# Optimization experiments

Measured on AMD Instinct MI355X. Metric: run time of the kernel, lower is better.

The kernel has to match this reference:

```python
import itertools
import jax, jax.numpy as jnp
import numpy as np

H, W = 512, 512
B, G, F, C = 2, 4, 9, 3
N = H * W


def _morton(pos):
    # pos: [N,3] int; interleave bits as in MortonFromPosition
    pos = np.asarray(pos, dtype=np.int32)
    code = np.zeros(len(pos), dtype=np.int64)
    coeff = np.asarray([4, 2, 1], dtype=np.int64)
    for b in range(21):
        code |= ((pos & (1 << b)) << (2 * b)) @ coeff
    return code


def _build_graph(h, w):
    xindex, yindex = np.meshgrid(np.arange(w), np.arange(h))
    xy = np.stack([yindex, xindex], axis=2).reshape(-1, 2)
    z = np.zeros((len(xy), 1), dtype=np.int64)
    hc = _morton(np.concatenate([xy, z], axis=1))
    order = np.argsort(hc)
    xy = xy[order]
    hc = hc[order]
    order_inv = np.zeros(len(xy), dtype=np.int32)
    order_inv[order] = np.arange(len(xy))
    deltas = np.array(list(itertools.product([-1, 0, 1], [-1, 0, 1])), dtype=np.int32)
    T = len(deltas)
    node_i = np.repeat(np.arange(len(xy), dtype=np.int32), T)
    loc_j = (xy[:, None, :] + deltas[None, :, :]).reshape(-1, 2)
    zc = np.zeros((len(loc_j), 1), dtype=np.int64)
    hj = _morton(np.concatenate([loc_j, zc], axis=1))
    pos = np.clip(np.searchsorted(hc, hj), 0, len(hc) - 1)
    valid = (hc[pos] == hj) & (loc_j[:, 0] >= 0) & (loc_j[:, 0] < h) \
            & (loc_j[:, 1] >= 0) & (loc_j[:, 1] < w)
    edges = np.stack([node_i[valid], pos[valid].astype(np.int32)], axis=1)
    return edges, order.astype(np.int32), order_inv


def setup_inputs() -> dict:
    key = jax.random.key(0)
    k1, k2, k3 = jax.random.split(key, 3)
    edges_np, order_np, order_inv_np = _build_graph(H, W)
    M_DIAG_INIT = 0.4
    multiM = jnp.eye(F, dtype=jnp.float32)[None, :, :] * M_DIAG_INIT
    multiM = jnp.tile(multiM, (G, 1, 1))
    return {
        "img_features": jax.random.normal(k1, (B, G, F, H, W), dtype=jnp.float32),
        "signals2d": jax.random.normal(k2, (B, G, C, H, W), dtype=jnp.float32),
        "multiM": multiM + 0.01 * jax.random.normal(k3, (G, F, F), dtype=jnp.float32),
        "edges": jnp.asarray(edges_np, dtype=jnp.int32),
        "order": jnp.asarray(order_np, dtype=jnp.int32),
        "order_inverse": jnp.asarray(order_inv_np, dtype=jnp.int32),
    }


def reference(img_features, signals2d, multiM, edges, order, order_inverse):
    b, g, f, h, w = img_features.shape
    n = h * w
    # F.normalize over feature dim (eps=1e-12)
    norm = jnp.sqrt(jnp.sum(img_features * img_features, axis=2, keepdims=True))
    feats = img_features / jnp.maximum(norm, 1e-12)
    # signal2D_to_graph_signals: flatten + Morton reorder
    node_feats = feats.reshape(b, g, f, n)[..., order]          # [b,g,f,n]
    fM = jnp.einsum('bgcn,gcv->bgvn', node_feats, multiM)        # [b,g,f,n]
    nodeI = edges[:, 0]
    nodeJ = edges[:, 1]
    sim = jnp.sum(fM[..., nodeI] * fM[..., nodeJ], axis=2)       # [b,g,E]
    ew = jnp.exp(jnp.clip(sim, -10.0, 10.0))                     # [b,g,E]
    # degree = scatter-add of edge weights by source node (== one-hot buffer sum)
    deg = jnp.zeros((b, g, n), dtype=ew.dtype).at[:, :, nodeI].add(ew)
    dinv = 1.0 / jnp.sqrt(deg)
    ew_n = dinv[:, :, nodeI] * ew * dinv[:, :, nodeJ]            # [b,g,E]
    # op_L_norm on graph signals
    sig = signals2d.reshape(b, g, -1, n)[..., order]             # [b,g,c,n]
    se = sig[..., nodeJ] * ew_n[:, :, None, :]                   # [b,g,c,E]
    agg = jnp.zeros_like(sig).at[:, :, :, nodeI].add(se)
    out = sig - agg
    # graph_signals_to_signal2D
    out2d = out[..., order_inverse].reshape(b, g, -1, h, w)
    return out2d
```

## Files before the change

### kernel.cpp

```cpp
#include <hip/hip_runtime.h>
#include <hip/hip_fp16.h>

#define Hh 512
#define Ww 512
#define Bb 2
#define Gg 4
#define Ff 9
#define Cc 3
#define Nn (Hh*Ww)

#define TILE 32
#define RS 36
#define RSP 37
#define DS 34
#define DSP 35
#define NT 256

struct __align__(16) FmVec { __half2 h[4]; };

struct FmPt { __half2 a0, a1, b0, b1; float cf; };

__device__ __forceinline__ float dotfm(const FmPt& p, const FmPt& q) {
    __half2 acc = __hmul2(p.a0, q.a0);
    acc = __hfma2(p.a1, q.a1, acc);
    acc = __hfma2(p.b0, q.b0, acc);
    acc = __hfma2(p.b1, q.b1, acc);
    return __low2float(acc) + __high2float(acc) + p.cf * q.cf;
}

__device__ __forceinline__ float ew_of(float s) { return __expf(s); }

__global__ void __launch_bounds__(NT, 5) fused_kernel(const float* __restrict__ img,
                                                      const float* __restrict__ M,
                                                      const float* __restrict__ sig,
                                                      float* __restrict__ out) {
    __shared__ FmVec  fmAB[RS * RSP];
    __shared__ __half fmC[RS * RSP];
    __shared__ __half dv[DS * DSP];

    const int tid = threadIdx.x;
    const int bg   = blockIdx.x & 7;
    const int tile = blockIdx.x >> 3;
    const int g    = bg & (Gg - 1);
    const int by0  = (tile >> 4) * TILE;
    const int bx0  = (tile & 15) * TILE;
    const bool border = (by0 == 0) | (by0 == Hh - TILE) | (bx0 == 0) | (bx0 == Ww - TILE);

    const float* imgP = img + (size_t)bg * Ff * Nn;
    const float* sgp  = sig + (size_t)bg * Cc * Nn;
    const float* Mg   = M + g * Ff * Ff;

    auto LD = [&](int idx) -> FmPt {
        FmPt p;
        FmVec v = fmAB[idx];
        p.a0 = v.h[0]; p.a1 = v.h[1]; p.b0 = v.h[2]; p.b1 = v.h[3];
        p.cf = __half2float(fmC[idx]);
        return p;
    };

    for (int i = tid; i < RS * RS; i += NT) {
        unsigned r = (unsigned)i / RS, c = (unsigned)i - r * RS;
        int gy = by0 - 2 + (int)r, gx = bx0 - 2 + (int)c;
        float m[Ff];
        if ((unsigned)gy < Hh && (unsigned)gx < Ww) {
            const float* src = imgP + gy * Ww + gx;
            float v[Ff]; float ss = 0.f;
#pragma unroll
            for (int f = 0; f < Ff; ++f) { v[f] = src[f * Nn]; ss += v[f] * v[f]; }
            float inv = 1.0f / fmaxf(sqrtf(ss), 1e-12f);
#pragma unroll
            for (int f = 0; f < Ff; ++f) v[f] *= inv;
#pragma unroll
            for (int vv = 0; vv < Ff; ++vv) {
                float acc = 0.f;
#pragma unroll
                for (int cc = 0; cc < Ff; ++cc) acc = fmaf(v[cc], Mg[cc * Ff + vv], acc);
                m[vv] = acc;
            }
        } else {
#pragma unroll
            for (int f = 0; f < Ff; ++f) m[f] = 0.f;
        }
        int si = r * RSP + c;
        FmVec vv;
        vv.h[0] = __floats2half2_rn(m[0], m[1]);
        vv.h[1] = __floats2half2_rn(m[2], m[3]);
        vv.h[2] = __floats2half2_rn(m[4], m[5]);
        vv.h[3] = __floats2half2_rn(m[6], m[7]);
        fmAB[si] = vv;
        fmC[si]  = __float2half_rn(m[8]);
    }
    __syncthreads();

    const int r2 = tid >> 4, c2 = tid & 15;
    const int gy0 = by0 + 2 * r2, gx0 = bx0 + 2 * c2;
    const int wb  = (2 * r2 + 1) * RSP + (2 * c2 + 1);

    FmPt w0[4], w1[4], w2[4], w3[4];
#pragma unroll
    for (int ci = 0; ci < 4; ++ci) w0[ci] = LD(wb + ci);
#pragma unroll
    for (int ci = 0; ci < 4; ++ci) w1[ci] = LD(wb + RSP + ci);
#pragma unroll
    for (int ci = 0; ci < 4; ++ci) w2[ci] = LD(wb + 2 * RSP + ci);

    float e0[9], e1[9], e2[9], e3[9];
    e0[0] = ew_of(dotfm(w1[1], w0[0])); e0[1] = ew_of(dotfm(w1[1], w0[1])); e0[2] = ew_of(dotfm(w1[1], w0[2]));
    e0[3] = ew_of(dotfm(w1[1], w1[0])); e0[4] = ew_of(dotfm(w1[1], w1[1])); e0[5] = ew_of(dotfm(w1[1], w1[2]));
    e0[6] = ew_of(dotfm(w1[1], w2[0])); e0[7] = ew_of(dotfm(w1[1], w2[1])); e0[8] = ew_of(dotfm(w1[1], w2[2]));
    e1[0] = ew_of(dotfm(w1[2], w0[1])); e1[1] = ew_of(dotfm(w1[2], w0[2])); e1[2] = ew_of(dotfm(w1[2], w0[3]));
    e1[3] = e0[5];                      e1[4] = ew_of(dotfm(w1[2], w1[2])); e1[5] = ew_of(dotfm(w1[2], w1[3]));
    e1[6] = ew_of(dotfm(w1[2], w2[1])); e1[7] = ew_of(dotfm(w1[2], w2[2])); e1[8] = ew_of(dotfm(w1[2], w2[3]));

#pragma unroll
    for (int ci = 0; ci < 4; ++ci) w3[ci] = LD(wb + 3 * RSP + ci);

    e2[0] = ew_of(dotfm(w2[1], w1[0])); e2[1] = e0[7];                      e2[2] = e1[6];
    e2[3] = ew_of(dotfm(w2[1], w2[0])); e2[4] = ew_of(dotfm(w2[1], w2[1])); e2[5] = ew_of(dotfm(w2[1], w2[2]));
    e2[6] = ew_of(dotfm(w2[1], w3[0])); e2[7] = ew_of(dotfm(w2[1], w3[1])); e2[8] = ew_of(dotfm(w2[1], w3[2]));
    e3[0] = e0[8];                      e3[1] = e1[7];                      e3[2] = ew_of(dotfm(w2[2], w1[3]));
    e3[3] = e2[5];                      e3[4] = ew_of(dotfm(w2[2], w2[2])); e3[5] = ew_of(dotfm(w2[2], w2[3]));
    e3[6] = ew_of(dotfm(w2[2], w3[1])); e3[7] = ew_of(dotfm(w2[2], w3[2])); e3[8] = ew_of(dotfm(w2[2], w3[3]));

    if (border) {
#pragma unroll
        for (int j = 0; j < 9; ++j) {
            int dy = j / 3 - 1, dx = j % 3 - 1;
            if (!(((unsigned)(gy0 + dy)     < Hh) & ((unsigned)(gx0 + dx)     < Ww))) e0[j] = 0.f;
            if (!(((unsigned)(gy0 + dy)     < Hh) & ((unsigned)(gx0 + 1 + dx) < Ww))) e1[j] = 0.f;
            if (!(((unsigned)(gy0 + 1 + dy) < Hh) & ((unsigned)(gx0 + dx)     < Ww))) e2[j] = 0.f;
            if (!(((unsigned)(gy0 + 1 + dy) < Hh) & ((unsigned)(gx0 + 1 + dx) < Ww))) e3[j] = 0.f;
        }
    }

    float deg0 = 0.f, deg1 = 0.f, deg2 = 0.f, deg3 = 0.f;
#pragma unroll
    for (int j = 0; j < 9; ++j) { deg0 += e0[j]; deg1 += e1[j]; deg2 += e2[j]; deg3 += e3[j]; }
    {
        const int db = (2 * r2 + 1) * DSP + (2 * c2 + 1);
        dv[db]           = __float2half_rn(1.0f / sqrtf(deg0));
        dv[db + 1]       = __float2half_rn(1.0f / sqrtf(deg1));
        dv[db + DSP]     = __float2half_rn(1.0f / sqrtf(deg2));
        dv[db + DSP + 1] = __float2half_rn(1.0f / sqrtf(deg3));
    }

    if (tid < 132) {
        int r, c;
        if (tid < 34)       { r = 0;        c = tid;       }
        else if (tid < 68)  { r = 33;       c = tid - 34;  }
        else if (tid < 100) { r = tid - 67; c = 0;         }
        else                { r = tid - 99; c = 33;        }
        int gy = by0 - 1 + r, gx = bx0 - 1 + c;
        float d = 1.0f;
        if ((unsigned)gy < Hh && (unsigned)gx < Ww) {
            int fi = (r + 1) * RSP + (c + 1);
            FmPt a = LD(fi);
            float deg = 0.f;
#pragma unroll
            for (int j = 0; j < 9; ++j) {
                int dy = j / 3 - 1, dx = j % 3 - 1;
                FmPt q = LD(fi + dy * RSP + dx);
                float e = ew_of(dotfm(a, q));
                bool valid = ((unsigned)(gy + dy) < Hh) & ((unsigned)(gx + dx) < Ww);
                deg += valid ? e : 0.f;
            }
            d = 1.0f / sqrtf(deg);
        }
        dv[r * DSP + c] = __float2half_rn(d);
    }
    __syncthreads();

    float dvf[16];
    {
        const int db = 2 * r2 * DSP + 2 * c2;
#pragma unroll
        for (int k = 0; k < 16; ++k)
            dvf[k] = __half2float(dv[db + (k >> 2) * DSP + (k & 3)]);
    }
    const float dp0 = dvf[5], dp1 = dvf[6], dp2 = dvf[9], dp3 = dvf[10];
#pragma unroll
    for (int j = 0; j < 9; ++j) {
        const int k0 = (j / 3) * 4 + (j % 3);
        e0[j] = dp0 * e0[j] * dvf[k0];
        e1[j] = dp1 * e1[j] * dvf[k0 + 1];
        e2[j] = dp2 * e2[j] * dvf[k0 + 4];
        e3[j] = dp3 * e3[j] * dvf[k0 + 5];
    }

    int ry[4], cx[4];
#pragma unroll
    for (int i = 0; i < 4; ++i) {
        ry[i] = min(max(gy0 - 1 + i, 0), Hh - 1) * Ww;
        cx[i] = min(max(gx0 - 1 + i, 0), Ww - 1);
    }

    float* o = out + (size_t)bg * Cc * Nn;
    const int p = gy0 * Ww + gx0;
#pragma unroll
    for (int ch = 0; ch < Cc; ++ch) {
        const float* sc = sgp + (size_t)ch * Nn;
        float s[16];
#pragma unroll
        for (int k = 0; k < 16; ++k) s[k] = sc[ry[k >> 2] + cx[k & 3]];
        float a0 = 0.f, a1 = 0.f, a2 = 0.f, a3 = 0.f;
#pragma unroll
        for (int j = 0; j < 9; ++j) {
            const int k0 = (j / 3) * 4 + (j % 3);
            a0 = fmaf(e0[j], s[k0],     a0);
            a1 = fmaf(e1[j], s[k0 + 1], a1);
            a2 = fmaf(e2[j], s[k0 + 4], a2);
            a3 = fmaf(e3[j], s[k0 + 5], a3);
        }
        float* oc = o + (size_t)ch * Nn;
        *(float2*)&oc[p]      = make_float2(s[5] - a0, s[6]  - a1);
        *(float2*)&oc[p + Ww] = make_float2(s[9] - a2, s[10] - a3);
    }
}

extern "C" void kernel_launch(void* const* d_in, const int* in_sizes, int n_in,
                              void* d_out, int out_size, void* d_ws, size_t ws_size,
                              hipStream_t stream) {
    const float* img = (const float*)d_in[0];
    const float* sig = (const float*)d_in[1];
    const float* M   = (const float*)d_in[2];
    float* out = (float*)d_out;

    fused_kernel<<<dim3(256 * Bb * Gg), NT, 0, stream>>>(img, M, sig, out);
}
```

Measured before the change: 36.94 us.

## Software-pipeline feature tile loads and prefetch signal channels before normalization barrier

The halo-tile fill loop now uses two register buffers, so the global loads for the next point are issued before the current point is normalized and projected. The normalization is folded into the matrix product with rsqrtf. Loads for signal channels 0 and 1 are hoisted above the degree-normalization step, and channel 2 is loaded before the aggregation, so global latency overlaps with other work. The cost is higher register pressure under launch_bounds(256,5), which could cause spills or lower occupancy.

```diff
diff --git a/kernel.cpp b/kernel.cpp
--- a/kernel.cpp
+++ b/kernel.cpp
@@ -58,30 +58,35 @@
         return p;
     };
 
-    for (int i = tid; i < RS * RS; i += NT) {
+    auto LOADPT = [&](float* v, int i, int& si, bool& inimg) {
         unsigned r = (unsigned)i / RS, c = (unsigned)i - r * RS;
         int gy = by0 - 2 + (int)r, gx = bx0 - 2 + (int)c;
+        si = (int)(r * RSP + c);
+        inimg = ((unsigned)gy < Hh) & ((unsigned)gx < Ww);
+        if (inimg) {
+            const float* src = imgP + gy * Ww + gx;
+#pragma unroll
+            for (int f = 0; f < Ff; ++f) v[f] = src[f * Nn];
+        }
+    };
+    auto PROCPT = [&](const float* v, int si, bool inimg) {
         float m[Ff];
-        if ((unsigned)gy < Hh && (unsigned)gx < Ww) {
-            const float* src = imgP + gy * Ww + gx;
-            float v[Ff]; float ss = 0.f;
-#pragma unroll
-            for (int f = 0; f < Ff; ++f) { v[f] = src[f * Nn]; ss += v[f] * v[f]; }
-            float inv = 1.0f / fmaxf(sqrtf(ss), 1e-12f);
-#pragma unroll
-            for (int f = 0; f < Ff; ++f) v[f] *= inv;
+        if (inimg) {
+            float ss = 0.f;
+#pragma unroll
+            for (int f = 0; f < Ff; ++f) ss = fmaf(v[f], v[f], ss);
+            float inv = rsqrtf(fmaxf(ss, 1e-24f));
 #pragma unroll
             for (int vv = 0; vv < Ff; ++vv) {
                 float acc = 0.f;
 #pragma unroll
                 for (int cc = 0; cc < Ff; ++cc) acc = fmaf(v[cc], Mg[cc * Ff + vv], acc);
-                m[vv] = acc;
+                m[vv] = acc * inv;
             }
         } else {
 #pragma unroll
             for (int f = 0; f < Ff; ++f) m[f] = 0.f;
         }
-        int si = r * RSP + c;
         FmVec vv;
         vv.h[0] = __floats2half2_rn(m[0], m[1]);
         vv.h[1] = __floats2half2_rn(m[2], m[3]);
@@ -89,6 +94,23 @@
         vv.h[3] = __floats2half2_rn(m[6], m[7]);
         fmAB[si] = vv;
         fmC[si]  = __float2half_rn(m[8]);
+    };
+
+    {
+        float vA[Ff], vB[Ff];
+        int siA = 0, siB = 0; bool okA = false, okB = false;
+        LOADPT(vA, tid, siA, okA);
+#pragma unroll
+        for (int k = 0; k < 6; k += 2) {
+            const int iB = tid + (k + 1) * NT;
+            const bool doB = iB < RS * RS;
+            if (doB) LOADPT(vB, iB, siB, okB);
+            PROCPT(vA, siA, okA);
+            const int iA2 = tid + (k + 2) * NT;
+            const bool doA2 = iA2 < RS * RS;
+            if (doA2) LOADPT(vA, iA2, siA, okA);
+            if (doB) PROCPT(vB, siB, okB);
+        }
     }
     __syncthreads();
 
@@ -170,6 +192,18 @@
     }
     __syncthreads();
 
+    int ry[4], cx[4];
+#pragma unroll
+    for (int i = 0; i < 4; ++i) {
+        ry[i] = min(max(gy0 - 1 + i, 0), Hh - 1) * Ww;
+        cx[i] = min(max(gx0 - 1 + i, 0), Ww - 1);
+    }
+    float s0[16], s1[16];
+#pragma unroll
+    for (int k = 0; k < 16; ++k) s0[k] = sgp[ry[k >> 2] + cx[k & 3]];
+#pragma unroll
+    for (int k = 0; k < 16; ++k) s1[k] = sgp[Nn + ry[k >> 2] + cx[k & 3]];
+
     float dvf[16];
     {
         const int db = 2 * r2 * DSP + 2 * c2;
@@ -187,33 +221,44 @@
         e3[j] = dp3 * e3[j] * dvf[k0 + 5];
     }
 
-    int ry[4], cx[4];
-#pragma unroll
-    for (int i = 0; i < 4; ++i) {
-        ry[i] = min(max(gy0 - 1 + i, 0), Hh - 1) * Ww;
-        cx[i] = min(max(gx0 - 1 + i, 0), Ww - 1);
-    }
+    float s2[16];
+#pragma unroll
+    for (int k = 0; k < 16; ++k) s2[k] = sgp[2 * Nn + ry[k >> 2] + cx[k & 3]];
 
     float* o = out + (size_t)bg * Cc * Nn;
     const int p = gy0 * Ww + gx0;
-#pragma unroll
-    for (int ch = 0; ch < Cc; ++ch) {
-        const float* sc = sgp + (size_t)ch * Nn;
-        float s[16];
-#pragma unroll
-        for (int k = 0; k < 16; ++k) s[k] = sc[ry[k >> 2] + cx[k & 3]];
+    {
         float a0 = 0.f, a1 = 0.f, a2 = 0.f, a3 = 0.f;
+        float b0 = 0.f, b1 = 0.f, b2 = 0.f, b3 = 0.f;
 #pragma unroll
         for (int j = 0; j < 9; ++j) {
             const int k0 = (j / 3) * 4 + (j % 3);
-            a0 = fmaf(e0[j], s[k0],     a0);
-            a1 = fmaf(e1[j], s[k0 + 1], a1);
-            a2 = fmaf(e2[j], s[k0 + 4], a2);
-            a3 = fmaf(e3[j], s[k0 + 5], a3);
-        }
-        float* oc = o + (size_t)ch * Nn;
-        *(float2*)&oc[p]      = make_float2(s[5] - a0, s[6]  - a1);
-        *(float2*)&oc[p + Ww] = make_float2(s[9] - a2, s[10] - a3);
+            a0 = fmaf(e0[j], s0[k0],     a0);
+            a1 = fmaf(e1[j], s0[k0 + 1], a1);
+            a2 = fmaf(e2[j], s0[k0 + 4], a2);
+            a3 = fmaf(e3[j], s0[k0 + 5], a3);
+            b0 = fmaf(e0[j], s1[k0],     b0);
+            b1 = fmaf(e1[j], s1[k0 + 1], b1);
+            b2 = fmaf(e2[j], s1[k0 + 4], b2);
+            b3 = fmaf(e3[j], s1[k0 + 5], b3);
+        }
+        *(float2*)&o[p]           = make_float2(s0[5] - a0, s0[6]  - a1);
+        *(float2*)&o[p + Ww]      = make_float2(s0[9] - a2, s0[10] - a3);
+        *(float2*)&o[Nn + p]      = make_float2(s1[5] - b0, s1[6]  - b1);
+        *(float2*)&o[Nn + p + Ww] = make_float2(s1[9] - b2, s1[10] - b3);
+    }
+    {
+        float c0 = 0.f, c1 = 0.f, c2v = 0.f, c3 = 0.f;
+#pragma unroll
+        for (int j = 0; j < 9; ++j) {
+            const int k0 = (j / 3) * 4 + (j % 3);
+            c0  = fmaf(e0[j], s2[k0],     c0);
+            c1  = fmaf(e1[j], s2[k0 + 1], c1);
+            c2v = fmaf(e2[j], s2[k0 + 4], c2v);
+            c3  = fmaf(e3[j], s2[k0 + 5], c3);
+        }
+        *(float2*)&o[2 * Nn + p]      = make_float2(s2[5] - c0,  s2[6]  - c1);
+        *(float2*)&o[2 * Nn + p + Ww] = make_float2(s2[9] - c2v, s2[10] - c3);
     }
 }
 
```

Result: faster. 36.10 us (-2.3%).
